# Kernel optimization log

Measured on AMD Instinct MI355X. Metric: run time of the kernel, lower is better.

Reference implementation:

```python
import jax, jax.numpy as jnp
import numpy as np

KERNEL_SIZE = 3

def setup_inputs() -> dict:
    key = jax.random.key(0)
    k1, k2, k3, k4, k5 = jax.random.split(key, 5)
    B, L, D, K = 4, 4096, 1024, KERNEL_SIZE
    x = jax.random.normal(k1, (B, L, D), dtype=jnp.float32)
    # depthwise conv: torch weight shape (D, 1, K) -> store as (D, K)
    fan_dw = 1.0 / np.sqrt(1 * K)
    w_dw = jax.random.uniform(k2, (D, K), dtype=jnp.float32, minval=-fan_dw, maxval=fan_dw)
    b_dw = jax.random.uniform(k3, (D,), dtype=jnp.float32, minval=-fan_dw, maxval=fan_dw)
    # pointwise conv: torch weight shape (D, D, 1) -> store as (D_out, D_in)
    fan_pw = 1.0 / np.sqrt(D * 1)
    w_pw = jax.random.uniform(k4, (D, D), dtype=jnp.float32, minval=-fan_pw, maxval=fan_pw)
    b_pw = jax.random.uniform(k5, (D,), dtype=jnp.float32, minval=-fan_pw, maxval=fan_pw)
    return {"x": x, "w_dw": w_dw, "b_dw": b_dw, "w_pw": w_pw, "b_pw": b_pw}

def _causal_dw_pw(x, w_dw, b_dw, w_pw, b_pw):
    # x: (B, L, D); causal left-pad by K-1 along L
    K = w_dw.shape[1]
    L = x.shape[1]
    xp = jnp.pad(x, ((0, 0), (K - 1, 0), (0, 0)))  # (B, L+K-1, D)
    # depthwise: y[b,l,d] = sum_k xp[b,l+k,d] * w_dw[d,k]
    y = sum(xp[:, k:k + L, :] * w_dw[:, k] for k in range(K)) + b_dw
    # pointwise 1x1 conv: mix channels
    return jnp.einsum('bld,ed->ble', y, w_pw) + b_pw

def reference(x, w_dw, b_dw, w_pw, b_pw):
    return _causal_dw_pw(x, w_dw, b_dw, w_pw, b_pw)
```

## Files before the change

### kernel.cpp

```cpp
#include <hip/hip_runtime.h>
#include <hip/hip_bf16.h>
#include <stdint.h>

#define B_SZ   4
#define L_SEQ  4096
#define D_DIM  1024
#define M_TOT  (B_SZ * L_SEQ)

typedef __bf16 bf16;
typedef __attribute__((ext_vector_type(8))) __bf16 bf16x8;
typedef __attribute__((ext_vector_type(4))) float   f32x4;

#define GLOAD_LDS16(g, l)                                                     \
  __builtin_amdgcn_global_load_lds(                                           \
      (const __attribute__((address_space(1))) void*)(g),                     \
      (__attribute__((address_space(3))) void*)(l), 16, 0, 0)

__global__ __launch_bounds__(256) void dw_bf16_kernel(
    const float* __restrict__ x, const float* __restrict__ w_dw,
    const float* __restrict__ b_dw, bf16* __restrict__ y,
    const float* __restrict__ w_pw, bf16* __restrict__ wpwb) {
  const int t = threadIdx.x;
  if (blockIdx.x >= B_SZ * (L_SEQ / 16)) {
    int i = ((blockIdx.x - B_SZ * (L_SEQ / 16)) * 256 + t) * 8;
    float4 a = *(const float4*)(w_pw + i);
    float4 b = *(const float4*)(w_pw + i + 4);
    union { bf16 h[8]; int4 v; } r;
    r.h[0] = (bf16)a.x; r.h[1] = (bf16)a.y; r.h[2] = (bf16)a.z; r.h[3] = (bf16)a.w;
    r.h[4] = (bf16)b.x; r.h[5] = (bf16)b.y; r.h[6] = (bf16)b.z; r.h[7] = (bf16)b.w;
    *(int4*)(wpwb + i) = r.v;
    return;
  }
  const int b  = blockIdx.x >> 8;
  const int l0 = (blockIdx.x & 255) * 16;
  const int d0 = t * 4;
  const float* xb = x + (size_t)b * L_SEQ * D_DIM + d0;
  bf16*        yb = y + (size_t)b * L_SEQ * D_DIM + d0;

  float4 xr[18];
  const float4 zero = make_float4(0.f, 0.f, 0.f, 0.f);
  xr[0] = (l0 >= 2) ? *(const float4*)(xb + (size_t)(l0 - 2) * D_DIM) : zero;
  xr[1] = (l0 >= 1) ? *(const float4*)(xb + (size_t)(l0 - 1) * D_DIM) : zero;
#pragma unroll
  for (int j = 0; j < 16; ++j)
    xr[j + 2] = *(const float4*)(xb + (size_t)(l0 + j) * D_DIM);

  const float* wp = w_dw + d0 * 3;
  float4 wa = *(const float4*)(wp);
  float4 wb = *(const float4*)(wp + 4);
  float4 wc = *(const float4*)(wp + 8);
  float4 bv = *(const float4*)(b_dw + d0);

#pragma unroll
  for (int j = 0; j < 16; ++j) {
    float4 x2 = xr[j], x1 = xr[j + 1], x0 = xr[j + 2];
    float a0 = fmaf(x2.x, wa.x, fmaf(x1.x, wa.y, fmaf(x0.x, wa.z, bv.x)));
    float a1 = fmaf(x2.y, wa.w, fmaf(x1.y, wb.x, fmaf(x0.y, wb.y, bv.y)));
    float a2 = fmaf(x2.z, wb.z, fmaf(x1.z, wb.w, fmaf(x0.z, wc.x, bv.z)));
    float a3 = fmaf(x2.w, wc.y, fmaf(x1.w, wc.z, fmaf(x0.w, wc.w, bv.w)));
    union { bf16 h[4]; int2 v; } o;
    o.h[0] = (bf16)a0; o.h[1] = (bf16)a1; o.h[2] = (bf16)a2; o.h[3] = (bf16)a3;
    *(int2*)(yb + (size_t)(l0 + j) * D_DIM) = o.v;
  }
}

#define BM 128
#define BN 128
#define BK 32
#define EP_ROWP 68

__global__ __launch_bounds__(256) void gemm_bt_kernel(
    const bf16* __restrict__ A,
    const bf16* __restrict__ Bm,
    const float* __restrict__ bias, float* __restrict__ C) {
  __shared__ __align__(16) char smem[32768];

  const int t    = threadIdx.x;
  const int m0   = blockIdx.x * BM;
  const int n0   = blockIdx.y * BN;
  const int lane = t & 63;
  const int wv   = t >> 6;
  const int wm   = (wv >> 1) * 64;
  const int wn   = (wv & 1) * 64;
  const int lrow = lane & 15;
  const int q    = lane >> 4;

  f32x4 acc[4][4] = {};

  int srow[2], sgc[2];
#pragma unroll
  for (int i = 0; i < 2; ++i) {
    int s   = i * 256 + t;
    srow[i] = s >> 2;
    sgc[i]  = (s & 3) ^ ((srow[i] >> 1) & 3);
  }
  const unsigned lbase = (unsigned)(wv * 1024);

  auto stage = [&](int p, int k0) {
#pragma unroll
    for (int i = 0; i < 2; ++i) {
      unsigned off = (unsigned)(p * 16384 + i * 4096) + lbase;
      GLOAD_LDS16(A  + (size_t)(m0 + srow[i]) * D_DIM + k0 + sgc[i] * 8, smem + off);
      GLOAD_LDS16(Bm + (size_t)(n0 + srow[i]) * D_DIM + k0 + sgc[i] * 8, smem + 8192 + off);
    }
  };

  stage(0, 0);
  for (int it = 0; it < D_DIM / BK; ++it) {
    __syncthreads();
    if (it < D_DIM / BK - 1) stage((it + 1) & 1, (it + 1) * BK);
    const char* Ab = smem + (it & 1) * 16384;
    const char* Bb = Ab + 8192;

    bf16x8 af[4], bfr[4];
#pragma unroll
    for (int i = 0; i < 4; ++i) {
      int mrow = wm + i * 16 + lrow;
      int ck   = q ^ ((mrow >> 1) & 3);
      af[i] = *(const bf16x8*)(Ab + (size_t)mrow * (BK * 2) + ck * 16);
      int nrow = wn + i * 16 + lrow;
      int ckb  = q ^ ((nrow >> 1) & 3);
      bfr[i] = *(const bf16x8*)(Bb + (size_t)nrow * (BK * 2) + ckb * 16);
    }
#pragma unroll
    for (int i = 0; i < 4; ++i)
#pragma unroll
      for (int j = 0; j < 4; ++j)
        acc[i][j] = __builtin_amdgcn_mfma_f32_16x16x32_bf16(af[i], bfr[j], acc[i][j], 0, 0, 0);
  }

  __syncthreads();
  float* ep = (float*)smem + (size_t)wv * (16 * EP_ROWP);

  float bvj[4];
#pragma unroll
  for (int j = 0; j < 4; ++j) bvj[j] = bias[n0 + wn + j * 16 + lrow];

#pragma unroll
  for (int i = 0; i < 4; ++i) {
#pragma unroll
    for (int j = 0; j < 4; ++j)
#pragma unroll
      for (int r = 0; r < 4; ++r)
        ep[(q * 4 + r) * EP_ROWP + j * 16 + lrow] = acc[i][j][r] + bvj[j];
#pragma unroll
    for (int it = 0; it < 4; ++it) {
      int flat = it * 64 + lane;
      int row  = flat >> 4;
      int c4   = flat & 15;
      float4 v = *(const float4*)(ep + row * EP_ROWP + c4 * 4);
      int gm = m0 + wm + i * 16 + row;
      int gn = n0 + wn + c4 * 4;
      *(float4*)(C + (size_t)gm * D_DIM + gn) = v;
    }
  }
}

__global__ __launch_bounds__(256) void fallback_kernel(
    const float* __restrict__ x, const float* __restrict__ w_dw,
    const float* __restrict__ b_dw, const float* __restrict__ w_pw,
    const float* __restrict__ b_pw, float* __restrict__ out) {
  __shared__ float ys[D_DIM];
  const int m = blockIdx.x;
  const int l = m & (L_SEQ - 1);
  const int t = threadIdx.x;
  const float* xr = x + (size_t)m * D_DIM;
#pragma unroll
  for (int c = 0; c < 4; ++c) {
    int d = t + c * 256;
    float a = fmaf(xr[d], w_dw[d * 3 + 2], b_dw[d]);
    if (l >= 1) a = fmaf(xr[d - D_DIM], w_dw[d * 3 + 1], a);
    if (l >= 2) a = fmaf(xr[d - 2 * D_DIM], w_dw[d * 3 + 0], a);
    ys[d] = a;
  }
  __syncthreads();
#pragma unroll
  for (int c = 0; c < 4; ++c) {
    int e = t + c * 256;
    const float* wr = w_pw + (size_t)e * D_DIM;
    float a = b_pw[e];
    for (int d = 0; d < D_DIM; ++d) a = fmaf(ys[d], wr[d], a);
    out[(size_t)m * D_DIM + e] = a;
  }
}

extern "C" void kernel_launch(void* const* d_in, const int* in_sizes, int n_in,
                              void* d_out, int out_size, void* d_ws, size_t ws_size,
                              hipStream_t stream) {
  (void)in_sizes; (void)n_in; (void)out_size;
  const float* x    = (const float*)d_in[0];
  const float* w_dw = (const float*)d_in[1];
  const float* b_dw = (const float*)d_in[2];
  const float* w_pw = (const float*)d_in[3];
  const float* b_pw = (const float*)d_in[4];
  float* out = (float*)d_out;

  const size_t y_elems = (size_t)M_TOT * D_DIM;
  const size_t w_elems = (size_t)D_DIM * D_DIM;
  const size_t need = (y_elems + w_elems) * sizeof(bf16);

  if (ws_size >= need) {
    bf16* y    = (bf16*)d_ws;
    bf16* wpwb = (bf16*)d_ws + y_elems;
    const int dw_blocks  = B_SZ * (L_SEQ / 16);
    const int cvt_blocks = (D_DIM * D_DIM / 8) / 256;
    dw_bf16_kernel<<<dw_blocks + cvt_blocks, 256, 0, stream>>>(x, w_dw, b_dw, y, w_pw, wpwb);
    dim3 grid(M_TOT / BM, D_DIM / BN);
    gemm_bt_kernel<<<grid, 256, 0, stream>>>(y, wpwb, b_pw, out);
  } else {
    fallback_kernel<<<M_TOT, 256, 0, stream>>>(x, w_dw, b_dw, w_pw, b_pw, out);
  }
}
```

Baseline: 168.2 us.

## Use BK=64 single-buffered GEMM with 8-chunk XOR swizzle and occupancy hint

```diff
diff --git a/kernel.cpp b/kernel.cpp
--- a/kernel.cpp
+++ b/kernel.cpp
@@ -66,10 +66,10 @@
 
 #define BM 128
 #define BN 128
-#define BK 32
+#define BK 64
 #define EP_ROWP 68
 
-__global__ __launch_bounds__(256) void gemm_bt_kernel(
+__global__ __launch_bounds__(256, 4) void gemm_bt_kernel(
     const bf16* __restrict__ A,
     const bf16* __restrict__ Bm,
     const float* __restrict__ bias, float* __restrict__ C) {
@@ -87,46 +87,54 @@
 
   f32x4 acc[4][4] = {};
 
-  int srow[2], sgc[2];
-#pragma unroll
-  for (int i = 0; i < 2; ++i) {
+  int goff[4];
+#pragma unroll
+  for (int i = 0; i < 4; ++i) {
     int s   = i * 256 + t;
-    srow[i] = s >> 2;
-    sgc[i]  = (s & 3) ^ ((srow[i] >> 1) & 3);
-  }
+    int row = s >> 3;
+    int gc  = (s & 7) ^ (row & 7);
+    goff[i] = row * (D_DIM * 2) + gc * 16;
+  }
+  const char* pA = (const char*)(A  + (size_t)m0 * D_DIM);
+  const char* pB = (const char*)(Bm + (size_t)n0 * D_DIM);
   const unsigned lbase = (unsigned)(wv * 1024);
 
-  auto stage = [&](int p, int k0) {
-#pragma unroll
-    for (int i = 0; i < 2; ++i) {
-      unsigned off = (unsigned)(p * 16384 + i * 4096) + lbase;
-      GLOAD_LDS16(A  + (size_t)(m0 + srow[i]) * D_DIM + k0 + sgc[i] * 8, smem + off);
-      GLOAD_LDS16(Bm + (size_t)(n0 + srow[i]) * D_DIM + k0 + sgc[i] * 8, smem + 8192 + off);
-    }
-  };
-
-  stage(0, 0);
+  int aoff[4], boff[4];
+#pragma unroll
+  for (int i = 0; i < 4; ++i) {
+    int mrow = wm + i * 16 + lrow;
+    aoff[i] = mrow * 128 + ((q ^ (mrow & 7)) * 16);
+    int nrow = wn + i * 16 + lrow;
+    boff[i] = 16384 + nrow * 128 + ((q ^ (nrow & 7)) * 16);
+  }
+
   for (int it = 0; it < D_DIM / BK; ++it) {
     __syncthreads();
-    if (it < D_DIM / BK - 1) stage((it + 1) & 1, (it + 1) * BK);
-    const char* Ab = smem + (it & 1) * 16384;
-    const char* Bb = Ab + 8192;
-
-    bf16x8 af[4], bfr[4];
 #pragma unroll
     for (int i = 0; i < 4; ++i) {
-      int mrow = wm + i * 16 + lrow;
-      int ck   = q ^ ((mrow >> 1) & 3);
-      af[i] = *(const bf16x8*)(Ab + (size_t)mrow * (BK * 2) + ck * 16);
-      int nrow = wn + i * 16 + lrow;
-      int ckb  = q ^ ((nrow >> 1) & 3);
-      bfr[i] = *(const bf16x8*)(Bb + (size_t)nrow * (BK * 2) + ckb * 16);
+      unsigned off = (unsigned)(i * 4096) + lbase;
+      GLOAD_LDS16(pA + goff[i], smem + off);
+      GLOAD_LDS16(pB + goff[i], smem + 16384 + off);
     }
-#pragma unroll
-    for (int i = 0; i < 4; ++i)
-#pragma unroll
-      for (int j = 0; j < 4; ++j)
-        acc[i][j] = __builtin_amdgcn_mfma_f32_16x16x32_bf16(af[i], bfr[j], acc[i][j], 0, 0, 0);
+    pA += BK * 2;
+    pB += BK * 2;
+    __syncthreads();
+
+#pragma unroll
+    for (int kk = 0; kk < 2; ++kk) {
+      const int x = kk * 64;
+      bf16x8 af[4], bfr[4];
+#pragma unroll
+      for (int i = 0; i < 4; ++i) {
+        af[i]  = *(const bf16x8*)(smem + (aoff[i] ^ x));
+        bfr[i] = *(const bf16x8*)(smem + (boff[i] ^ x));
+      }
+#pragma unroll
+      for (int i = 0; i < 4; ++i)
+#pragma unroll
+        for (int j = 0; j < 4; ++j)
+          acc[i][j] = __builtin_amdgcn_mfma_f32_16x16x32_bf16(af[i], bfr[j], acc[i][j], 0, 0, 0);
+    }
   }
 
   __syncthreads();
@@ -144,8 +152,8 @@
       for (int r = 0; r < 4; ++r)
         ep[(q * 4 + r) * EP_ROWP + j * 16 + lrow] = acc[i][j][r] + bvj[j];
 #pragma unroll
-    for (int it = 0; it < 4; ++it) {
-      int flat = it * 64 + lane;
+    for (int s = 0; s < 4; ++s) {
+      int flat = s * 64 + lane;
       int row  = flat >> 4;
       int c4   = flat & 15;
       float4 v = *(const float4*)(ep + row * EP_ROWP + c4 * 4);
```

New measurement: 173.5 us. 1.03x slower.
